# Optimization experiments

Hardware: AMD Instinct MI355X
Metric: run time of the kernel (lower is better)

## Reference

```python
import jax, jax.numpy as jnp
import numpy as np

B, S, D, H = 4, 2048, 1024, 16
DH = D // H  # per-head dim = 64


def setup_inputs() -> dict:
    key = jax.random.key(0)
    ks = jax.random.split(key, 7)
    s_in = 1.0 / np.sqrt(D)
    return {
        "x": jax.random.normal(ks[0], (B, S, D), dtype=jnp.float32),
        "Wq": jax.random.normal(ks[1], (H, D, DH), dtype=jnp.float32) * s_in,
        "bq": jnp.zeros((H, DH), dtype=jnp.float32),
        "Wk": jax.random.normal(ks[2], (H, D, DH), dtype=jnp.float32) * s_in,
        "bk": jnp.zeros((H, DH), dtype=jnp.float32),
        "Wv": jax.random.normal(ks[3], (H, D, DH), dtype=jnp.float32) * s_in,
        "bv": jnp.zeros((H, DH), dtype=jnp.float32),
    }


def reference(x, Wq, bq, Wk, bk, Wv, bv):
    # Batched form of the per-head Python loop: all heads in one einsum.
    q = jnp.einsum("bsd,hde->bhse", x, Wq) + bq[None, :, None, :]
    k = jnp.einsum("bsd,hde->bhse", x, Wk) + bk[None, :, None, :]
    v = jnp.einsum("bsd,hde->bhse", x, Wv) + bv[None, :, None, :]
    scale = 1.0 / jnp.sqrt(jnp.asarray(DH, dtype=q.dtype))
    scores = jnp.einsum("bhse,bhte->bhst", q, k) * scale  # [B,H,S,S]
    attn = jax.nn.softmax(scores, axis=-1)
    out = jnp.einsum("bhst,bhte->bhse", attn, v)  # [B,H,S,DH]
    # concat heads along last dim (head order preserved, as torch.cat)
    return out.transpose(0, 2, 1, 3).reshape(B, S, H * DH)
```

## Files before the change

kernel.cpp:

```cpp
#include <hip/hip_runtime.h>
#include <cstdint>
#include <cstddef>

#define B_   4
#define S_   2048
#define D_   1024
#define H_   16
#define DH_  64

typedef __attribute__((ext_vector_type(8))) short short8;
typedef __attribute__((ext_vector_type(4))) float f32x4;

#define SWZ16(row, ch) ((((row) * 8) + (((ch) ^ ((row) & 7)))) * 8)

static __device__ __forceinline__ unsigned short f2b(float f){
    unsigned int u = __float_as_uint(f);
    return (unsigned short)((u + 0x7FFFu + ((u >> 16) & 1u)) >> 16);
}
static __device__ __forceinline__ unsigned int cvtpk(float lo, float hi){
    unsigned int r;
    asm("v_cvt_pk_bf16_f32 %0, %1, %2" : "=v"(r) : "v"(lo), "v"(hi));
    return r;
}
static __device__ __forceinline__ float exp2_hw(float x){
    float r;
    asm("v_exp_f32 %0, %1" : "=v"(r) : "v"(x));
    return r;
}

__global__ __launch_bounds__(256)
void cvt_x_kernel(const float* __restrict__ x, unsigned short* __restrict__ xb){
    size_t i0 = ((size_t)blockIdx.x * 256 + threadIdx.x) * 8;
    float4 a = *(const float4*)(x + i0);
    float4 b = *(const float4*)(x + i0 + 4);
    union { unsigned short u[8]; uint4 v; } r;
    r.u[0]=f2b(a.x); r.u[1]=f2b(a.y); r.u[2]=f2b(a.z); r.u[3]=f2b(a.w);
    r.u[4]=f2b(b.x); r.u[5]=f2b(b.y); r.u[6]=f2b(b.z); r.u[7]=f2b(b.w);
    *(uint4*)(xb + i0) = r.v;
}

__global__ __launch_bounds__(256)
void cvt_w_kernel(const float* __restrict__ Wq, const float* __restrict__ Wk,
                  const float* __restrict__ Wv, unsigned short* __restrict__ wt){
    int id = blockIdx.x * 256 + threadIdx.x;
    int e4 = (id & 15) * 4;
    int k  = (id >> 4) & 1023;
    int h  = (id >> 14) & 15;
    int t_ = id >> 18;
    const float* W = (t_ == 0) ? Wq : ((t_ == 1) ? Wk : Wv);
    float4 w = *(const float4*)(W + (((size_t)h * D_ + k) * DH_ + e4));
    unsigned short* dst = wt + (((size_t)t_ * H_ + h) * DH_ + e4) * D_ + k;
    dst[0]            = f2b(w.x);
    dst[(size_t)D_]   = f2b(w.y);
    dst[(size_t)2*D_] = f2b(w.z);
    dst[(size_t)3*D_] = f2b(w.w);
}

__global__ __launch_bounds__(256)
void qkv_proj_mfma(const unsigned short* __restrict__ xb,
                   const unsigned short* __restrict__ wtg,
                   const float* __restrict__ bq, const float* __restrict__ bk,
                   const float* __restrict__ bv,
                   unsigned short* __restrict__ qb,
                   unsigned short* __restrict__ kb,
                   unsigned short* __restrict__ vt)
{
    const int mb  = blockIdx.x;
    const int h   = blockIdx.y;
    const int t   = threadIdx.x;
    const int w   = t >> 6;
    const int l   = t & 63;
    const int l15 = l & 15;
    const int g   = l >> 4;
    const int wm  = w >> 1;
    const int wn  = w & 1;

    __shared__ unsigned short xs[128 * 64];
    __shared__ unsigned short ws[192 * 64];
    __shared__ float bias_s[192];

    if (t < 192){
        int tensor = t >> 6, eloc = t & 63;
        const float* bp = (tensor == 0) ? bq : ((tensor == 1) ? bk : bv);
        bias_s[t] = bp[h * DH_ + eloc];
    }

    f32x4 acc[4][6];
#pragma unroll
    for (int mt = 0; mt < 4; ++mt)
#pragma unroll
        for (int nt = 0; nt < 6; ++nt) acc[mt][nt] = (f32x4){0.f,0.f,0.f,0.f};

    const int m0 = mb * 128;

    const int rowx = t >> 3, chx = t & 7;
    int xlo[4], wlo[6];
    const unsigned short* wpt[6];
#pragma unroll
    for (int it = 0; it < 4; ++it) xlo[it] = SWZ16(rowx + 32*it, chx);
#pragma unroll
    for (int it = 0; it < 6; ++it){
        int row = rowx + 32*it;
        wlo[it] = SWZ16(row, chx);
        wpt[it] = wtg + (((size_t)(row >> 6) * H_ + h) * DH_ + (row & 63)) * D_ + chx*8;
    }
    const unsigned short* xp = xb + (size_t)(m0 + rowx) * D_ + chx*8;

    short8 xR[4], wR[6];
#pragma unroll
    for (int it = 0; it < 4; ++it) xR[it] = *(const short8*)(xp + (size_t)it*32*D_);
#pragma unroll
    for (int it = 0; it < 6; ++it) wR[it] = *(const short8*)(wpt[it]);

    for (int k0 = 0; k0 < D_; k0 += 64){
        __syncthreads();
#pragma unroll
        for (int it = 0; it < 4; ++it) *(short8*)&xs[xlo[it]] = xR[it];
#pragma unroll
        for (int it = 0; it < 6; ++it) *(short8*)&ws[wlo[it]] = wR[it];
        if (k0 + 64 < D_){
#pragma unroll
            for (int it = 0; it < 4; ++it)
                xR[it] = *(const short8*)(xp + (size_t)it*32*D_ + k0 + 64);
#pragma unroll
            for (int it = 0; it < 6; ++it)
                wR[it] = *(const short8*)(wpt[it] + k0 + 64);
        }
        __syncthreads();

#pragma unroll
        for (int ks = 0; ks < 2; ++ks){
            short8 a[4];
#pragma unroll
            for (int mt = 0; mt < 4; ++mt)
                a[mt] = *(const short8*)&xs[SWZ16(64*wm + 16*mt + l15, 4*ks + g)];
#pragma unroll
            for (int nt = 0; nt < 6; ++nt){
                short8 bb = *(const short8*)&ws[SWZ16(96*wn + 16*nt + l15, 4*ks + g)];
#pragma unroll
                for (int mt = 0; mt < 4; ++mt)
                    acc[mt][nt] = __builtin_amdgcn_mfma_f32_16x16x32_bf16(a[mt], bb, acc[mt][nt], 0,0,0);
            }
        }
    }

    const float QSCALE = 0.180336880f;
    const int b   = m0 >> 11;
    const int bh  = b * H_ + h;
    const int sbase = (m0 & (S_ - 1)) + 64 * wm;
#pragma unroll
    for (int mt = 0; mt < 4; ++mt){
        int s0 = sbase + 16 * mt + 4 * g;
#pragma unroll
        for (int ntl = 0; ntl < 6; ++ntl){
            int nt = 6 * wn + ntl;
            float bias = bias_s[16 * nt + l15];
            if (nt < 4){
                int e = 16 * nt + l15;
                size_t base = ((size_t)bh * S_ + s0) * DH_ + e;
#pragma unroll
                for (int r = 0; r < 4; ++r)
                    qb[base + (size_t)r * DH_] = f2b((acc[mt][ntl][r] + bias) * QSCALE);
            } else if (nt < 8){
                int e = 16 * (nt - 4) + l15;
                size_t base = ((size_t)bh * S_ + s0) * DH_ + e;
#pragma unroll
                for (int r = 0; r < 4; ++r)
                    kb[base + (size_t)r * DH_] = f2b(acc[mt][ntl][r] + bias);
            } else {
                int e = 16 * (nt - 8) + l15;
                union { unsigned short u[4]; uint2 v; } pk;
#pragma unroll
                for (int r = 0; r < 4; ++r) pk.u[r] = f2b(acc[mt][ntl][r] + bias);
                *(uint2*)(vt + ((size_t)bh * DH_ + e) * S_ + s0) = pk.v;
            }
        }
    }
}

__global__ __launch_bounds__(256)
void attn_mfma(const unsigned short* __restrict__ qb,
               const unsigned short* __restrict__ kb,
               const unsigned short* __restrict__ vt,
               float* __restrict__ out)
{
    const int qt  = blockIdx.x;
    const int bh  = blockIdx.y;
    const int b   = bh >> 4, h = bh & 15;
    const int t   = threadIdx.x;
    const int w   = t >> 6;
    const int l   = t & 63;
    const int l15 = l & 15;
    const int g   = l >> 4;

    __shared__ unsigned short Kl [64 * 64];
    __shared__ unsigned short Vtl[64 * 64];
    __shared__ unsigned short Pl [4 * 16 * 64];
    unsigned short* Pw = Pl + w * 16 * 64;

    const size_t bhb = (size_t)bh * S_ * DH_;

    short8 qf[2];
    {
        const int qrow = qt * 64 + 16 * w + l15;
        const unsigned short* qp = qb + bhb + (size_t)qrow * DH_ + g * 8;
        qf[0] = *(const short8*)(qp);
        qf[1] = *(const short8*)(qp + 32);
    }

    const short8 ones8 = {(short)0x3F80,(short)0x3F80,(short)0x3F80,(short)0x3F80,
                          (short)0x3F80,(short)0x3F80,(short)0x3F80,(short)0x3F80};

    f32x4 o[4], lacc;
#pragma unroll
    for (int nt = 0; nt < 4; ++nt) o[nt] = (f32x4){0.f,0.f,0.f,0.f};
    lacc = (f32x4){0.f,0.f,0.f,0.f};

    const int row0 = t >> 3, ch0 = t & 7;
    const int klo0 = SWZ16(row0, ch0), klo1 = SWZ16(row0 + 32, ch0);
    const unsigned short* kp0 = kb + bhb + (size_t)row0 * DH_ + ch0 * 8;
    const unsigned short* kp1 = kp0 + (size_t)32 * DH_;
    const unsigned short* vp0 = vt + bhb + (size_t)row0 * S_ + ch0 * 8;
    const unsigned short* vp1 = vp0 + (size_t)32 * S_;

    short8 ka0, ka1, va0, va1, kb0, kb1, vb0, vb1;
    ka0 = *(const short8*)kp0; ka1 = *(const short8*)kp1;
    va0 = *(const short8*)vp0; va1 = *(const short8*)vp1;
    kp0 += 64*DH_; kp1 += 64*DH_; vp0 += 64; vp1 += 64;

    auto compute_tile = [&](){
        f32x4 st[4];
#pragma unroll
        for (int mt = 0; mt < 4; ++mt) st[mt] = (f32x4){0.f,0.f,0.f,0.f};
        __builtin_amdgcn_s_setprio(1);
#pragma unroll
        for (int ks = 0; ks < 2; ++ks)
#pragma unroll
            for (int mt = 0; mt < 4; ++mt){
                short8 ak = *(const short8*)&Kl[SWZ16(16*mt + l15, 4*ks + g)];
                st[mt] = __builtin_amdgcn_mfma_f32_16x16x32_bf16(ak, qf[ks], st[mt], 0,0,0);
            }
        __builtin_amdgcn_s_setprio(0);
#pragma unroll
        for (int mt = 0; mt < 4; ++mt){
            uint2 pp;
            pp.x = cvtpk(exp2_hw(st[mt][0] - 16.f), exp2_hw(st[mt][1] - 16.f));
            pp.y = cvtpk(exp2_hw(st[mt][2] - 16.f), exp2_hw(st[mt][3] - 16.f));
            int pc = 2*mt + (g >> 1);
            *(uint2*)(Pw + (l15 * 8 + (pc ^ (l15 & 7))) * 8 + (g & 1) * 4) = pp;
        }
        asm volatile("s_waitcnt lgkmcnt(0)" ::: "memory");
        __builtin_amdgcn_sched_barrier(0);
        __builtin_amdgcn_s_setprio(1);
#pragma unroll
        for (int ks = 0; ks < 2; ++ks){
            short8 ap = *(const short8*)&Pw[SWZ16(l15, 4*ks + g)];
            lacc = __builtin_amdgcn_mfma_f32_16x16x32_bf16(ap, ones8, lacc, 0,0,0);
#pragma unroll
            for (int nt = 0; nt < 4; ++nt){
                short8 bv2 = *(const short8*)&Vtl[SWZ16(16*nt + l15, 4*ks + g)];
                o[nt] = __builtin_amdgcn_mfma_f32_16x16x32_bf16(ap, bv2, o[nt], 0,0,0);
            }
        }
        __builtin_amdgcn_s_setprio(0);
    };

    for (int kt = 0; kt < S_ / 64; kt += 2){
        __syncthreads();
        *(short8*)&Kl [klo0] = ka0; *(short8*)&Kl [klo1] = ka1;
        *(short8*)&Vtl[klo0] = va0; *(short8*)&Vtl[klo1] = va1;
        kb0 = *(const short8*)kp0; kb1 = *(const short8*)kp1;
        vb0 = *(const short8*)vp0; vb1 = *(const short8*)vp1;
        kp0 += 64*DH_; kp1 += 64*DH_; vp0 += 64; vp1 += 64;
        __syncthreads();
        compute_tile();

        __syncthreads();
        *(short8*)&Kl [klo0] = kb0; *(short8*)&Kl [klo1] = kb1;
        *(short8*)&Vtl[klo0] = vb0; *(short8*)&Vtl[klo1] = vb1;
        if (kt + 2 < S_ / 64){
            ka0 = *(const short8*)kp0; ka1 = *(const short8*)kp1;
            va0 = *(const short8*)vp0; va1 = *(const short8*)vp1;
            kp0 += 64*DH_; kp1 += 64*DH_; vp0 += 64; vp1 += 64;
        }
        __syncthreads();
        compute_tile();
    }

    float invl[4];
#pragma unroll
    for (int r = 0; r < 4; ++r) invl[r] = 1.f / lacc[r];
    const int srow0 = qt * 64 + 16 * w + 4 * g;
#pragma unroll
    for (int nt = 0; nt < 4; ++nt)
#pragma unroll
        for (int r = 0; r < 4; ++r)
            out[((size_t)b * S_ + srow0 + r) * D_ + h * DH_ + 16 * nt + l15] =
                o[nt][r] * invl[r];
}

extern "C" void kernel_launch(void* const* d_in, const int* in_sizes, int n_in,
                              void* d_out, int out_size, void* d_ws, size_t ws_size,
                              hipStream_t stream) {
    const float* x  = (const float*)d_in[0];
    const float* Wq = (const float*)d_in[1];
    const float* bq = (const float*)d_in[2];
    const float* Wk = (const float*)d_in[3];
    const float* bk = (const float*)d_in[4];
    const float* Wv = (const float*)d_in[5];
    const float* bv = (const float*)d_in[6];
    float* out = (float*)d_out;

    char* wsp = (char*)d_ws;
    unsigned short* xb  = (unsigned short*)(wsp);
    unsigned short* wtg = (unsigned short*)(wsp + 16777216);
    unsigned short* qb  = (unsigned short*)(wsp + 23068672);
    unsigned short* kb  = (unsigned short*)(wsp + 39845888);
    unsigned short* vt  = (unsigned short*)(wsp + 56623104);

    cvt_x_kernel<<<4096, 256, 0, stream>>>(x, xb);
    cvt_w_kernel<<<3072, 256, 0, stream>>>(Wq, Wk, Wv, wtg);
    qkv_proj_mfma<<<dim3(64, 16), 256, 0, stream>>>(xb, wtg, bq, bk, bv, qb, kb, vt);
    attn_mfma<<<dim3(32, 64), 256, 0, stream>>>(qb, kb, vt, out);
}
```

Before: 296.5 us.

## Use direct global-to-LDS loads with double-buffered LDS in projection and attention

Both the QKV projection GEMM and the attention kernel stop staging tiles through registers. They now use global_load_lds (16-byte) into double-buffered shared memory, so the next tile's load overlaps the current tile's MFMA work and each iteration needs one barrier instead of two. The attention grid is flattened to 1D with a block-index swizzle that spreads neighbouring blocks across batch-heads, likely aimed at cache or XCD locality. Doubling LDS raises shared memory per block, which may lower occupancy, and the XOR swizzle is now applied on the global-address side.

Result: no change. 300.6 us (+1.4%).

```diff
diff --git a/kernel.cpp b/kernel.cpp
--- a/kernel.cpp
+++ b/kernel.cpp
@@ -26,6 +26,10 @@
     float r;
     asm("v_exp_f32 %0, %1" : "=v"(r) : "v"(x));
     return r;
+}
+static __device__ __forceinline__ void gl2lds16(const unsigned short* g, unsigned short* l){
+    __builtin_amdgcn_global_load_lds((const __attribute__((address_space(1))) void*)g,
+                                     (__attribute__((address_space(3))) void*)l, 16, 0, 0);
 }
 
 __global__ __launch_bounds__(256)
@@ -75,8 +79,8 @@
     const int wm  = w >> 1;
     const int wn  = w & 1;
 
-    __shared__ unsigned short xs[128 * 64];
-    __shared__ unsigned short ws[192 * 64];
+    __shared__ unsigned short xs [2][128 * 64];
+    __shared__ unsigned short ws2[2][192 * 64];
     __shared__ float bias_s[192];
 
     if (t < 192){
@@ -93,55 +97,54 @@
 
     const int m0 = mb * 128;
 
-    const int rowx = t >> 3, chx = t & 7;
-    int xlo[4], wlo[6];
-    const unsigned short* wpt[6];
-#pragma unroll
-    for (int it = 0; it < 4; ++it) xlo[it] = SWZ16(rowx + 32*it, chx);
-#pragma unroll
-    for (int it = 0; it < 6; ++it){
-        int row = rowx + 32*it;
-        wlo[it] = SWZ16(row, chx);
-        wpt[it] = wtg + (((size_t)(row >> 6) * H_ + h) * DH_ + (row & 63)) * D_ + chx*8;
-    }
-    const unsigned short* xp = xb + (size_t)(m0 + rowx) * D_ + chx*8;
-
-    short8 xR[4], wR[6];
-#pragma unroll
-    for (int it = 0; it < 4; ++it) xR[it] = *(const short8*)(xp + (size_t)it*32*D_);
-#pragma unroll
-    for (int it = 0; it < 6; ++it) wR[it] = *(const short8*)(wpt[it]);
+    const int rl = l >> 3;
+    const int cl = (l & 7) ^ (rl & 7);
+    const unsigned short* xg[4];
+    const unsigned short* wg[6];
+#pragma unroll
+    for (int i = 0; i < 4; ++i){
+        int row = (4*w + i) * 8 + rl;
+        xg[i] = xb + (size_t)(m0 + row) * D_ + cl * 8;
+    }
+#pragma unroll
+    for (int j = 0; j < 6; ++j){
+        int row = (6*w + j) * 8 + rl;
+        wg[j] = wtg + (((size_t)(row >> 6) * H_ + h) * DH_ + (row & 63)) * D_ + cl * 8;
+    }
+
+    auto stage = [&](int buf, int k0){
+#pragma unroll
+        for (int i = 0; i < 4; ++i)
+            gl2lds16(xg[i] + k0, &xs[buf][(4*w + i) * 512]);
+#pragma unroll
+        for (int j = 0; j < 6; ++j)
+            gl2lds16(wg[j] + k0, &ws2[buf][(6*w + j) * 512]);
+    };
+
+    stage(0, 0);
+    asm volatile("s_waitcnt vmcnt(0)" ::: "memory");
+    __syncthreads();
+    int cur = 0;
 
     for (int k0 = 0; k0 < D_; k0 += 64){
-        __syncthreads();
-#pragma unroll
-        for (int it = 0; it < 4; ++it) *(short8*)&xs[xlo[it]] = xR[it];
-#pragma unroll
-        for (int it = 0; it < 6; ++it) *(short8*)&ws[wlo[it]] = wR[it];
-        if (k0 + 64 < D_){
-#pragma unroll
-            for (int it = 0; it < 4; ++it)
-                xR[it] = *(const short8*)(xp + (size_t)it*32*D_ + k0 + 64);
-#pragma unroll
-            for (int it = 0; it < 6; ++it)
-                wR[it] = *(const short8*)(wpt[it] + k0 + 64);
-        }
-        __syncthreads();
-
+        if (k0 + 64 < D_) stage(cur ^ 1, k0 + 64);
 #pragma unroll
         for (int ks = 0; ks < 2; ++ks){
             short8 a[4];
 #pragma unroll
             for (int mt = 0; mt < 4; ++mt)
-                a[mt] = *(const short8*)&xs[SWZ16(64*wm + 16*mt + l15, 4*ks + g)];
+                a[mt] = *(const short8*)&xs[cur][SWZ16(64*wm + 16*mt + l15, 4*ks + g)];
 #pragma unroll
             for (int nt = 0; nt < 6; ++nt){
-                short8 bb = *(const short8*)&ws[SWZ16(96*wn + 16*nt + l15, 4*ks + g)];
+                short8 bb = *(const short8*)&ws2[cur][SWZ16(96*wn + 16*nt + l15, 4*ks + g)];
 #pragma unroll
                 for (int mt = 0; mt < 4; ++mt)
                     acc[mt][nt] = __builtin_amdgcn_mfma_f32_16x16x32_bf16(a[mt], bb, acc[mt][nt], 0,0,0);
             }
         }
+        asm volatile("s_waitcnt vmcnt(0)" ::: "memory");
+        __syncthreads();
+        cur ^= 1;
     }
 
     const float QSCALE = 0.180336880f;
@@ -184,8 +187,10 @@
                const unsigned short* __restrict__ vt,
                float* __restrict__ out)
 {
-    const int qt  = blockIdx.x;
-    const int bh  = blockIdx.y;
+    const int bid = blockIdx.x;
+    const int swz = (bid & 7) * 256 + (bid >> 3);
+    const int qt  = swz & 31;
+    const int bh  = swz >> 5;
     const int b   = bh >> 4, h = bh & 15;
     const int t   = threadIdx.x;
     const int w   = t >> 6;
@@ -193,10 +198,10 @@
     const int l15 = l & 15;
     const int g   = l >> 4;
 
-    __shared__ unsigned short Kl [64 * 64];
-    __shared__ unsigned short Vtl[64 * 64];
-    __shared__ unsigned short Pl [4 * 16 * 64];
-    unsigned short* Pw = Pl + w * 16 * 64;
+    __shared__ unsigned short Kl[2][64 * 64];
+    __shared__ unsigned short Vl[2][64 * 64];
+    __shared__ unsigned short Pl[4][16 * 64];
+    unsigned short* Pw = Pl[w];
 
     const size_t bhb = (size_t)bh * S_ * DH_;
 
@@ -216,19 +221,29 @@
     for (int nt = 0; nt < 4; ++nt) o[nt] = (f32x4){0.f,0.f,0.f,0.f};
     lacc = (f32x4){0.f,0.f,0.f,0.f};
 
-    const int row0 = t >> 3, ch0 = t & 7;
-    const int klo0 = SWZ16(row0, ch0), klo1 = SWZ16(row0 + 32, ch0);
-    const unsigned short* kp0 = kb + bhb + (size_t)row0 * DH_ + ch0 * 8;
-    const unsigned short* kp1 = kp0 + (size_t)32 * DH_;
-    const unsigned short* vp0 = vt + bhb + (size_t)row0 * S_ + ch0 * 8;
-    const unsigned short* vp1 = vp0 + (size_t)32 * S_;
-
-    short8 ka0, ka1, va0, va1, kb0, kb1, vb0, vb1;
-    ka0 = *(const short8*)kp0; ka1 = *(const short8*)kp1;
-    va0 = *(const short8*)vp0; va1 = *(const short8*)vp1;
-    kp0 += 64*DH_; kp1 += 64*DH_; vp0 += 64; vp1 += 64;
-
-    auto compute_tile = [&](){
+    const int rl = l >> 3;
+    const int cl = (l & 7) ^ (rl & 7);
+    const int sA = 2 * w, sB = 2 * w + 1;
+    const unsigned short* kgA = kb + bhb + (size_t)(sA*8 + rl) * DH_ + cl*8;
+    const unsigned short* kgB = kb + bhb + (size_t)(sB*8 + rl) * DH_ + cl*8;
+    const unsigned short* vgA = vt + bhb + (size_t)(sA*8 + rl) * S_  + cl*8;
+    const unsigned short* vgB = vt + bhb + (size_t)(sB*8 + rl) * S_  + cl*8;
+
+    auto stage = [&](int buf, int kt){
+        gl2lds16(kgA + (size_t)kt * 64 * DH_, &Kl[buf][sA * 512]);
+        gl2lds16(kgB + (size_t)kt * 64 * DH_, &Kl[buf][sB * 512]);
+        gl2lds16(vgA + kt * 64,               &Vl[buf][sA * 512]);
+        gl2lds16(vgB + kt * 64,               &Vl[buf][sB * 512]);
+    };
+
+    stage(0, 0);
+    asm volatile("s_waitcnt vmcnt(0)" ::: "memory");
+    __syncthreads();
+    int cur = 0;
+
+    for (int kt = 0; kt < S_ / 64; ++kt){
+        if (kt + 1 < S_ / 64) stage(cur ^ 1, kt + 1);
+
         f32x4 st[4];
 #pragma unroll
         for (int mt = 0; mt < 4; ++mt) st[mt] = (f32x4){0.f,0.f,0.f,0.f};
@@ -237,10 +252,11 @@
         for (int ks = 0; ks < 2; ++ks)
 #pragma unroll
             for (int mt = 0; mt < 4; ++mt){
-                short8 ak = *(const short8*)&Kl[SWZ16(16*mt + l15, 4*ks + g)];
+                short8 ak = *(const short8*)&Kl[cur][SWZ16(16*mt + l15, 4*ks + g)];
                 st[mt] = __builtin_amdgcn_mfma_f32_16x16x32_bf16(ak, qf[ks], st[mt], 0,0,0);
             }
         __builtin_amdgcn_s_setprio(0);
+
 #pragma unroll
         for (int mt = 0; mt < 4; ++mt){
             uint2 pp;
@@ -251,6 +267,7 @@
         }
         asm volatile("s_waitcnt lgkmcnt(0)" ::: "memory");
         __builtin_amdgcn_sched_barrier(0);
+
         __builtin_amdgcn_s_setprio(1);
 #pragma unroll
         for (int ks = 0; ks < 2; ++ks){
@@ -258,33 +275,15 @@
             lacc = __builtin_amdgcn_mfma_f32_16x16x32_bf16(ap, ones8, lacc, 0,0,0);
 #pragma unroll
             for (int nt = 0; nt < 4; ++nt){
-                short8 bv2 = *(const short8*)&Vtl[SWZ16(16*nt + l15, 4*ks + g)];
+                short8 bv2 = *(const short8*)&Vl[cur][SWZ16(16*nt + l15, 4*ks + g)];
                 o[nt] = __builtin_amdgcn_mfma_f32_16x16x32_bf16(ap, bv2, o[nt], 0,0,0);
             }
         }
         __builtin_amdgcn_s_setprio(0);
-    };
-
-    for (int kt = 0; kt < S_ / 64; kt += 2){
+
+        asm volatile("s_waitcnt vmcnt(0)" ::: "memory");
         __syncthreads();
-        *(short8*)&Kl [klo0] = ka0; *(short8*)&Kl [klo1] = ka1;
-        *(short8*)&Vtl[klo0] = va0; *(short8*)&Vtl[klo1] = va1;
-        kb0 = *(const short8*)kp0; kb1 = *(const short8*)kp1;
-        vb0 = *(const short8*)vp0; vb1 = *(const short8*)vp1;
-        kp0 += 64*DH_; kp1 += 64*DH_; vp0 += 64; vp1 += 64;
-        __syncthreads();
-        compute_tile();
-
-        __syncthreads();
-        *(short8*)&Kl [klo0] = kb0; *(short8*)&Kl [klo1] = kb1;
-        *(short8*)&Vtl[klo0] = vb0; *(short8*)&Vtl[klo1] = vb1;
-        if (kt + 2 < S_ / 64){
-            ka0 = *(const short8*)kp0; ka1 = *(const short8*)kp1;
-            va0 = *(const short8*)vp0; va1 = *(const short8*)vp1;
-            kp0 += 64*DH_; kp1 += 64*DH_; vp0 += 64; vp1 += 64;
-        }
-        __syncthreads();
-        compute_tile();
+        cur ^= 1;
     }
 
     float invl[4];
@@ -321,5 +320,5 @@
     cvt_x_kernel<<<4096, 256, 0, stream>>>(x, xb);
     cvt_w_kernel<<<3072, 256, 0, stream>>>(Wq, Wk, Wv, wtg);
     qkv_proj_mfma<<<dim3(64, 16), 256, 0, stream>>>(xb, wtg, bq, bk, bv, qb, kb, vt);
-    attn_mfma<<<dim3(32, 64), 256, 0, stream>>>(qb, kb, vt, out);
-}
+    attn_mfma<<<2048, 256, 0, stream>>>(qb, kb, vt, out);
+}
```
